# Kernel optimization log

Hardware: AMD Instinct MI355X
Metric: run time of the kernel (lower is better)

Reference implementation:

```python
import jax, jax.numpy as jnp
import numpy as np

N_HOS, N_TYP, N_STRUCTS = 2, 3, 8
N_COMBOS = N_HOS * N_TYP  # 6
BATCH = 32768
N_ITERS = 150  # PDHG iterations to solve the per-sample QP

S_NP = np.array([[1,0,0,1,0,1,0,0],
                 [0,1,0,1,0,0,1,0],
                 [0,0,1,0,1,0,0,1],
                 [1,0,0,0,1,1,0,0],
                 [0,1,0,0,0,0,1,1],
                 [0,0,1,1,1,0,0,0]], dtype=np.float32)


def setup_inputs() -> dict:
    key = jax.random.key(0)
    ks = jax.random.split(key, 10)
    def lin(kw, fan_in, fan_out):
        lim = 1.0 / np.sqrt(fan_in)
        kw1, kw2 = jax.random.split(kw)
        W = jax.random.uniform(kw1, (fan_out, fan_in), jnp.float32, -lim, lim)
        b = jax.random.uniform(kw2, (fan_out,), jnp.float32, -lim, lim)
        return W, b
    W1, b1 = lin(ks[0], 6, 20)
    W2, b2 = lin(ks[1], 20, 20)
    W3, b3 = lin(ks[2], 20, 20)
    W4, b4 = lin(ks[3], 20, 8)
    X = jax.random.uniform(ks[4], (BATCH, N_HOS, N_TYP), jnp.float32)  # nonneg bids -> feasible QP (x=0)
    return {"X": X, "W1": W1, "b1": b1, "W2": W2, "b2": b2, "W3": W3, "b3": b3,
            "W4": W4, "b4": b4, "S": jnp.asarray(S_NP), "batch_size": BATCH}


def _solve_qp(z, b, S):
    """Batched PDHG for: max w.x - ||x-z||_2  s.t. x>=0, S x <= b, with w = 1.
    z: [B, ns], b: [B, m], S: [m, ns]. Returns x: [B, ns]."""
    B, ns = z.shape
    m = S.shape[0]
    w = jnp.ones_like(z)
    # K = [S; -I]; Frobenius bound on spectral norm (safe step sizes)
    L = jnp.sqrt(jnp.sum(S * S) + ns)
    tau = 0.9 / L
    sigma = 0.9 / L

    def prox_f(u):
        # prox of tau*(||x-z|| - w.x) at u  (closed form: shifted norm shrinkage)
        v = u + tau * w - z
        nv = jnp.linalg.norm(v, axis=-1, keepdims=True)
        scale = jnp.maximum(1.0 - tau / jnp.maximum(nv, 1e-12), 0.0)
        return z + scale * v

    def step(carry, _):
        x, l1, l2 = carry
        x_new = prox_f(x - tau * (l1 @ S - l2))  # K^T lam = S^T l1 - l2
        xbar = 2.0 * x_new - x
        l1n = jnp.maximum(l1 + sigma * (xbar @ S.T) - sigma * b, 0.0)  # dual of Sx<=b
        l2n = jnp.maximum(l2 - sigma * xbar, 0.0)                      # dual of -x<=0
        return (x_new, l1n, l2n), None

    x0 = jnp.maximum(z, 0.0)
    l1 = jnp.zeros((B, m), z.dtype)
    l2 = jnp.zeros((B, ns), z.dtype)
    (x, _, _), _ = jax.lax.scan(step, (x0, l1, l2), None, length=N_ITERS)
    return x


def reference(X, W1, b1, W2, b2, W3, b3, W4, b4, S, batch_size):
    B = X.shape[0]
    Z = X.reshape(B, -1)                       # [B, 6] = bids flattened (also the QP rhs b)
    h = jnp.tanh(Z @ W1.T + b1)
    h = jnp.tanh(h @ W2.T + b2)
    h = jnp.tanh(h @ W3.T + b3)
    z = jnp.tanh(h @ W4.T + b4)                # [B, 8] anchor point for QP
    return _solve_qp(z, Z, S)                  # [B, 8] allocation
```

## Files before the change

### kernel.cpp

```cpp
#include <hip/hip_runtime.h>
#include <math.h>


#define NITERS 150

typedef float v2 __attribute__((ext_vector_type(2)));

__device__ __forceinline__ v2 vfma(v2 a, v2 b, v2 c) {
    return __builtin_elementwise_fma(a, b, c);
}
__device__ __forceinline__ v2 vmax(v2 a, v2 b) {
    return __builtin_elementwise_max(a, b);
}
#define LD2(W, off) (*(const v2*)((W) + (off)))

__device__ __forceinline__ float ftanh(float a) {
    float e = __expf(2.0f * a);
    return fmaf(-2.0f, __builtin_amdgcn_rcpf(e + 1.0f), 1.0f);
}

template<int P0, int P1, int P2, int P3>
__device__ __forceinline__ float qp(float x) {
    constexpr int ctrl = P0 | (P1 << 2) | (P2 << 4) | (P3 << 6);
    int xi = __builtin_bit_cast(int, x);
    int yi = __builtin_amdgcn_update_dpp(0, xi, ctrl, 0xF, 0xF, true);
    return __builtin_bit_cast(float, yi);
}

#define FOR20(M) M(0) M(1) M(2) M(3) M(4) M(5) M(6) M(7) M(8) M(9) \
                 M(10) M(11) M(12) M(13) M(14) M(15) M(16) M(17) M(18) M(19)
#define FOR8(M)  M(0) M(1) M(2) M(3) M(4) M(5) M(6) M(7)

#define PK20(W, base, H) \
  ( vfma(LD2(W,(base)+0),H##0, vfma(LD2(W,(base)+4),H##2, vfma(LD2(W,(base)+8),H##4, \
      vfma(LD2(W,(base)+12),H##6, LD2(W,(base)+16)*H##8)))) \
  + vfma(LD2(W,(base)+2),H##1, vfma(LD2(W,(base)+6),H##3, vfma(LD2(W,(base)+10),H##5, \
      vfma(LD2(W,(base)+14),H##7, LD2(W,(base)+18)*H##9)))) )

#define PACK10(P, t) \
  v2 P##0 = {t##_0,  t##_1},  P##1 = {t##_2,  t##_3},  P##2 = {t##_4,  t##_5}; \
  v2 P##3 = {t##_6,  t##_7},  P##4 = {t##_8,  t##_9},  P##5 = {t##_10, t##_11}; \
  v2 P##6 = {t##_12, t##_13}, P##7 = {t##_14, t##_15}, P##8 = {t##_16, t##_17}; \
  v2 P##9 = {t##_18, t##_19};

__global__ __launch_bounds__(256, 2)
void matchnet_kernel(
    const float* __restrict__ X,
    const float* __restrict__ W1, const float* __restrict__ b1,
    const float* __restrict__ W2, const float* __restrict__ b2,
    const float* __restrict__ W3, const float* __restrict__ b3,
    const float* __restrict__ W4, const float* __restrict__ b4,
    float* __restrict__ out, int B)
{
    const int tid = blockIdx.x * 256 + threadIdx.x;
    const int s   = tid >> 2;
    if (s >= B) return;
    const int g   = tid & 3;

    const float TAU = 0.9f / sqrtf(26.0f);
    const float SIG = TAU;
    const float TS  = TAU * SIG;

    float zin0, zin1, zin2, zin3, zin4, zin5;
    v2 zin01, zin23, zin45;
    {
        const float2* xp = (const float2*)(X + (size_t)s * 6);
        float2 p0 = xp[0], p1 = xp[1], p2 = xp[2];
        zin0 = p0.x; zin1 = p0.y; zin2 = p1.x;
        zin3 = p1.y; zin4 = p2.x; zin5 = p2.y;
        zin01 = (v2){p0.x, p0.y}; zin23 = (v2){p1.x, p1.y}; zin45 = (v2){p2.x, p2.y};
    }

#define L1R(j) float t1_##j; { \
        v2 r_ = vfma(LD2(W1,(j)*6+0), zin01, vfma(LD2(W1,(j)*6+2), zin23, LD2(W1,(j)*6+4)*zin45)); \
        t1_##j = ftanh(b1[j] + (r_.x + r_.y)); }
    FOR20(L1R)
    PACK10(A, t1)
#define L2R(j) float t2_##j; { \
        v2 r_ = PK20(W2, (j)*20, A); \
        t2_##j = ftanh(b2[j] + (r_.x + r_.y)); }
    FOR20(L2R)
    PACK10(Bh, t2)
#define L3R(j) float t3_##j; { \
        v2 r_ = PK20(W3, (j)*20, Bh); \
        t3_##j = ftanh(b3[j] + (r_.x + r_.y)); }
    FOR20(L3R)
    PACK10(C, t3)
#define ZR(j) float z##j; { \
        v2 r_ = PK20(W4, (j)*20, C); \
        z##j = ftanh(b4[j] + (r_.x + r_.y)); }
    FOR8(ZR)

    const bool b0 = (g & 1), b1_ = (g & 2);
    float z01 = b0 ? z1 : z0,  z23 = b0 ? z3 : z2;
    float zA  = b1_ ? z23 : z01;
    float z45 = b0 ? z5 : z4,  z67 = b0 ? z7 : z6;
    float zB  = b1_ ? z67 : z45;

    float i01 = b0 ? zin1 : zin0, i23 = b0 ? zin3 : zin2;
    float igA = b1_ ? i23 : i01;
    float i45 = b0 ? zin5 : zin4;
    float sbA = SIG * igA;
    float sbB = (g < 2) ? SIG * i45 : 1e30f;

    v2 zv = {zA, zB};
    v2 w  = {zA + zA - fmaxf(zA, 0.0f), zB + zB - fmaxf(zB, 0.0f)};
    v2 q  = {0.0f, 0.0f};
    v2 p  = {fmaxf(-zA, 0.0f) + TAU, fmaxf(-zB, 0.0f) + TAU};
    float lA = 0.0f, lB = 0.0f;

    const v2 vTAU  = {TAU, TAU};
    const v2 vmTAU = {-TAU, -TAU};
    const v2 vmTS  = {-TS, -TS};
    const v2 vTWO  = {2.0f, 2.0f};
    const v2 vZERO = {0.0f, 0.0f};

#pragma unroll 1
    for (int it = 0; it < NITERS; ++it) {
        float gA1  = qp<0,1,2,0>(lA);
        float gA2a = qp<3,0,0,1>(lA);
        float gA2b = qp<0,0,1,0>(lB);
        float gA2  = ((g == 0) || (g == 3)) ? gA2a : gA2b;
        float gA3  = qp<2,2,2,1>(lB);
        float stA = (gA1 + gA2) + gA3;
        float gB1  = qp<2,0,1,2>(lA);
        float gB2a = qp<3,3,0,0>(lA);
        float gB2b = qp<0,0,0,0>(lB);
        float gB2  = (g < 2) ? gB2a : gB2b;
        float gB3  = qp<1,2,2,2>(lB);
        float stB = (gB1 + gB2) + gB3;

        v2 st = {stA, stB};
        v2 v  = vfma(vmTAU, st, p);

        v2 sq = v * v;
        float nl = sq.x + sq.y;
        nl = nl + qp<1,0,3,2>(nl);
        nl = nl + qp<2,3,0,1>(nl);
        float scale = fmaxf(fmaf(-TAU, __builtin_amdgcn_rsqf(nl), 1.0f), 0.0f);
        v2 vscale = {scale, scale};

        v2 sv = vscale * v;
        v2 xb = vfma(vTWO, sv, w);
        w = zv - sv;
        q = vmax(vfma(vmTS, xb, q), vZERO);
        p = (sv + q) + vTAU;

        float xbA = xb.x, xbB = xb.y;

        float h1  = qp<0,1,2,0>(xbA);
        float h2a = qp<3,3,0,0>(xbA);
        float h2b = qp<0,0,0,0>(xbB);
        float h2  = (g < 2) ? h2a : h2b;
        float h3  = qp<1,2,3,1>(xbB);
        float rA = (h1 + h2) + h3;
        float k1  = qp<1,2,0,0>(xbA);
        float k2a = qp<0,3,0,0>(xbA);
        float k2b = qp<2,0,0,0>(xbB);
        float k2  = (g == 1) ? k2a : k2b;
        float k3  = qp<3,0,0,0>(xbB);
        float rB = (k1 + k2) + k3;

        lA = fmaxf(fmaf(SIG, rA, lA) - sbA, 0.0f);
        lB = fmaxf(fmaf(SIG, rB, lB) - sbB, 0.0f);
    }

    out[(size_t)s * 8 + g]     = zA + zA - w.x;
    out[(size_t)s * 8 + 4 + g] = zB + zB - w.y;
}

extern "C" void kernel_launch(void* const* d_in, const int* in_sizes, int n_in,
                              void* d_out, int out_size, void* d_ws, size_t ws_size,
                              hipStream_t stream) {
    const float* X  = (const float*)d_in[0];
    const float* W1 = (const float*)d_in[1];
    const float* b1 = (const float*)d_in[2];
    const float* W2 = (const float*)d_in[3];
    const float* b2 = (const float*)d_in[4];
    const float* W3 = (const float*)d_in[5];
    const float* b3 = (const float*)d_in[6];
    const float* W4 = (const float*)d_in[7];
    const float* b4 = (const float*)d_in[8];
    float* out = (float*)d_out;
    const int B = in_sizes[0] / 6;
    const int threads = B * 4;
    const int blocks = (threads + 255) / 256;
    hipLaunchKernelGGL(matchnet_kernel, dim3(blocks), dim3(256), 0, stream,
                       X, W1, b1, W2, b2, W3, b3, W4, b4, out, B);
}
```

Measured before the change: 111.5 us.

## Use linearity of S to gather v before norm, shortening PDHG critical path

Restructures each PDHG iteration so the S-row gather of the dual update runs on v (the pre-scale vector) in parallel with the norm reduction, exploiting S·(scale·v) = scale·S·v. The dual update becomes a single fma after scale is known, and running S·w terms are tracked incrementally. The DPP intrinsic's old operand is also changed to the source value instead of zero. This removes the serial dependence of the DPP gather on the rsqrt result and trades a few extra registers and FMAs for a shorter loop-carried latency chain.

```diff
diff --git a/kernel.cpp b/kernel.cpp
--- a/kernel.cpp
+++ b/kernel.cpp
@@ -23,7 +23,7 @@
 __device__ __forceinline__ float qp(float x) {
     constexpr int ctrl = P0 | (P1 << 2) | (P2 << 4) | (P3 << 6);
     int xi = __builtin_bit_cast(int, x);
-    int yi = __builtin_amdgcn_update_dpp(0, xi, ctrl, 0xF, 0xF, true);
+    int yi = __builtin_amdgcn_update_dpp(xi, xi, ctrl, 0xF, 0xF, true);
     return __builtin_bit_cast(float, yi);
 }
 
@@ -42,6 +42,20 @@
   v2 P##3 = {t##_6,  t##_7},  P##4 = {t##_8,  t##_9},  P##5 = {t##_10, t##_11}; \
   v2 P##6 = {t##_12, t##_13}, P##7 = {t##_14, t##_15}, P##8 = {t##_16, t##_17}; \
   v2 P##9 = {t##_18, t##_19};
+
+#define SROW_GATHER(aA, aB, outA, outB, g_) \
+    float h1_ = qp<0,1,2,0>(aA); \
+    float h2a_ = qp<3,3,0,0>(aA); \
+    float h2b_ = qp<0,0,0,0>(aB); \
+    float h2_ = ((g_) < 2) ? h2a_ : h2b_; \
+    float h3_ = qp<1,2,3,1>(aB); \
+    float outA = (h1_ + h2_) + h3_; \
+    float k1_ = qp<1,2,0,0>(aA); \
+    float k2a_ = qp<0,3,0,0>(aA); \
+    float k2b_ = qp<2,0,0,0>(aB); \
+    float k2_ = ((g_) == 1) ? k2a_ : k2b_; \
+    float k3_ = qp<3,0,0,0>(aB); \
+    float outB = (k1_ + k2_) + k3_;
 
 __global__ __launch_bounds__(256, 2)
 void matchnet_kernel(
@@ -60,6 +74,7 @@
     const float TAU = 0.9f / sqrtf(26.0f);
     const float SIG = TAU;
     const float TS  = TAU * SIG;
+    const float SIG2 = 2.0f * SIG;
 
     float zin0, zin1, zin2, zin3, zin4, zin5;
     v2 zin01, zin23, zin45;
@@ -104,13 +119,20 @@
     float sbB = (g < 2) ? SIG * i45 : 1e30f;
 
     v2 zv = {zA, zB};
-    v2 w  = {zA + zA - fmaxf(zA, 0.0f), zB + zB - fmaxf(zB, 0.0f)};
+    v2 sv = {fmaxf(zA, 0.0f) - zA, fmaxf(zB, 0.0f) - zB};
+    v2 svt = {sv.x + TAU, sv.y + TAU};
     v2 q  = {0.0f, 0.0f};
-    v2 p  = {fmaxf(-zA, 0.0f) + TAU, fmaxf(-zB, 0.0f) + TAU};
+    v2 w  = {zv.x - sv.x, zv.y - sv.y};
     float lA = 0.0f, lB = 0.0f;
 
+    float SzrA, SzrB, Ssv0A, Ssv0B;
+    { SROW_GATHER(zA, zB, oA, oB, g)  SzrA = oA; SzrB = oB; }
+    { SROW_GATHER(sv.x, sv.y, oA, oB, g)  Ssv0A = oA; Ssv0B = oB; }
+    float SwrA = SzrA - Ssv0A, SwrB = SzrB - Ssv0B;
+    float HA = fmaf(SIG, SwrA, -sbA);
+    float HB = fmaf(SIG, SwrB, -sbB);
+
     const v2 vTAU  = {TAU, TAU};
-    const v2 vmTAU = {-TAU, -TAU};
     const v2 vmTS  = {-TS, -TS};
     const v2 vTWO  = {2.0f, 2.0f};
     const v2 vZERO = {0.0f, 0.0f};
@@ -122,47 +144,43 @@
         float gA2b = qp<0,0,1,0>(lB);
         float gA2  = ((g == 0) || (g == 3)) ? gA2a : gA2b;
         float gA3  = qp<2,2,2,1>(lB);
-        float stA = (gA1 + gA2) + gA3;
+        float sABA = gA1 + gA2;
         float gB1  = qp<2,0,1,2>(lA);
         float gB2a = qp<3,3,0,0>(lA);
         float gB2b = qp<0,0,0,0>(lB);
         float gB2  = (g < 2) ? gB2a : gB2b;
         float gB3  = qp<1,2,2,2>(lB);
-        float stB = (gB1 + gB2) + gB3;
-
-        v2 st = {stA, stB};
-        v2 v  = vfma(vmTAU, st, p);
+        float sABB = gB1 + gB2;
+
+        float vA = fmaf(-TAU, sABA, svt.x) + fmaf(-TAU, gA3, q.x);
+        float vB = fmaf(-TAU, sABB, svt.y) + fmaf(-TAU, gB3, q.y);
+        v2 v = {vA, vB};
+
+        SROW_GATHER(vA, vB, SvrA, SvrB, g)
+        float GA = SIG2 * SvrA;
+        float GB = SIG2 * SvrB;
 
         v2 sq = v * v;
         float nl = sq.x + sq.y;
         nl = nl + qp<1,0,3,2>(nl);
         nl = nl + qp<2,3,0,1>(nl);
         float scale = fmaxf(fmaf(-TAU, __builtin_amdgcn_rsqf(nl), 1.0f), 0.0f);
-        v2 vscale = {scale, scale};
-
-        v2 sv = vscale * v;
-        v2 xb = vfma(vTWO, sv, w);
-        w = zv - sv;
-        q = vmax(vfma(vmTS, xb, q), vZERO);
-        p = (sv + q) + vTAU;
-
-        float xbA = xb.x, xbB = xb.y;
-
-        float h1  = qp<0,1,2,0>(xbA);
-        float h2a = qp<3,3,0,0>(xbA);
-        float h2b = qp<0,0,0,0>(xbB);
-        float h2  = (g < 2) ? h2a : h2b;
-        float h3  = qp<1,2,3,1>(xbB);
-        float rA = (h1 + h2) + h3;
-        float k1  = qp<1,2,0,0>(xbA);
-        float k2a = qp<0,3,0,0>(xbA);
-        float k2b = qp<2,0,0,0>(xbB);
-        float k2  = (g == 1) ? k2a : k2b;
-        float k3  = qp<3,0,0,0>(xbB);
-        float rB = (k1 + k2) + k3;
-
-        lA = fmaxf(fmaf(SIG, rA, lA) - sbA, 0.0f);
-        lB = fmaxf(fmaf(SIG, rB, lB) - sbB, 0.0f);
+
+        lA = fmaxf(fmaf(scale, GA, HA), 0.0f);
+        lB = fmaxf(fmaf(scale, GB, HB), 0.0f);
+
+        SwrA = fmaf(-scale, SvrA, SzrA);
+        SwrB = fmaf(-scale, SvrB, SzrB);
+        HA = fmaf(SIG, SwrA, lA - sbA);
+        HB = fmaf(SIG, SwrB, lB - sbB);
+
+        v2 vs = {scale, scale};
+        v2 svn = vs * v;
+        v2 xb  = vfma(vTWO, svn, w);
+        w  = zv - svn;
+        q  = vmax(vfma(vmTS, xb, q), vZERO);
+        sv = svn;
+        svt = svn + vTAU;
     }
 
     out[(size_t)s * 8 + g]     = zA + zA - w.x;
```

Result: no change. 113.2 us (+1.4%).
